# Kernel tuning notes

Hardware: AMD Instinct MI355X
Metric: run time of the kernel (lower is better)

Reference implementation:

```python
import jax, jax.numpy as jnp
import numpy as np

K = 8  # kNN fan-in (includes self at distance 0, matching torch_cluster.knn)


def _mlp2(x, w1, b1, w2, b2):
    # PyG MLP with plain_last=True: act between layers, none after last
    h = jax.nn.relu(x @ w1 + b1)
    return h @ w2 + b2


def _dynamic_edge_conv(x, w1, b1, w2, b2, k=K):
    # x: [B, N, C]. Recompute kNN graph from current features, EdgeConv with
    # message = MLP([x_i, x_j - x_i]) and max aggregation over neighbors.
    sq = jnp.sum(x * x, axis=-1)                                   # [B, N]
    d2 = sq[:, :, None] + sq[:, None, :] - 2.0 * jnp.einsum('bnc,bmc->bnm', x, x)
    _, idx = jax.lax.top_k(-d2, k)                                 # [B, N, k]
    xj = jax.vmap(lambda xx, ii: xx[ii])(x, idx)                   # [B, N, k, C]
    xi = jnp.broadcast_to(x[:, :, None, :], xj.shape)
    e = jnp.concatenate([xi, xj - xi], axis=-1)                    # [B, N, k, 2C]
    msg = _mlp2(e, w1, b1, w2, b2)                                 # [B, N, k, C_out]
    return jnp.max(msg, axis=2)                                    # [B, N, C_out]


def setup_inputs() -> dict:
    key = jax.random.key(0)
    ks = jax.random.split(key, 24)
    B, N = 2, 1000
    S = 0.05
    p = lambda i, shape: jax.random.normal(ks[i], shape, jnp.float32) * S
    return dict(
        pos=jax.random.normal(ks[0], (B, N, 3), jnp.float32),
        c1_w1=p(1, (6, 16)),   c1_b1=p(2, (16,)),  c1_w2=p(3, (16, 32)),   c1_b2=p(4, (32,)),
        c2_w1=p(5, (64, 64)),  c2_b1=p(6, (64,)),  c2_w2=p(7, (64, 128)),  c2_b2=p(8, (128,)),
        c3_w1=p(9, (256, 256)), c3_b1=p(10, (256,)), c3_w2=p(11, (256, 512)), c3_b2=p(12, (512,)),
        sm_w1=p(13, (672, 256)), sm_b1=p(14, (256,)), sm_w2=p(15, (256, 128)), sm_b2=p(16, (128,)),
        ec_w1=p(17, (384, 128)), ec_b1=p(18, (128,)), ec_w2=p(19, (128, 1)), ec_b2=p(20, (1,)),
    )


def reference(pos, c1_w1, c1_b1, c1_w2, c1_b2, c2_w1, c2_b1, c2_w2, c2_b2,
              c3_w1, c3_b1, c3_w2, c3_b2, sm_w1, sm_b1, sm_w2, sm_b2,
              ec_w1, ec_b1, ec_w2, ec_b2):
    x1 = _dynamic_edge_conv(pos, c1_w1, c1_b1, c1_w2, c1_b2)       # [B, N, 32]
    x2 = _dynamic_edge_conv(x1, c2_w1, c2_b1, c2_w2, c2_b2)        # [B, N, 128]
    x3 = _dynamic_edge_conv(x2, c3_w1, c3_b1, c3_w2, c3_b2)        # [B, N, 512]
    x = jnp.concatenate([x1, x2, x3], axis=-1)                     # [B, N, 672]
    sf = _mlp2(x, sm_w1, sm_b1, sm_w2, sm_b2)                      # [B, N, 128]
    g = jnp.max(sf, axis=1)                                        # [B, 128] global max pool

    N = pos.shape[1]
    t0, t1 = np.triu_indices(N, 1)                                 # 499500 pairs
    D = sf.shape[-1]
    # Linear(cat[feat_i, feat_j, global]) split into three small GEMMs on
    # [B,N,128] / [B,128] then gathered to pairs: identical math, avoids the
    # [B, P, 384] concat the torch code materializes.
    hi = sf @ ec_w1[:D]                                            # [B, N, 128]
    hj = sf @ ec_w1[D:2 * D]                                       # [B, N, 128]
    hg = g @ ec_w1[2 * D:] + ec_b1                                 # [B, 128]
    hidden = jax.nn.relu(hi[:, t0] + hj[:, t1] + hg[:, None, :])   # [B, P, 128]
    mlp_out = (hidden @ ec_w2 + ec_b2)[..., 0]                     # [B, P]
    pair_prob = jax.nn.sigmoid(mlp_out)
    return pair_prob, mlp_out
```

## Files before the change

kernel.cpp:

```cpp
#include <hip/hip_runtime.h>
#include <hip/hip_bf16.h>
#include <cmath>

#define NB 2
#define NP 1000
#define KNN 8
#define PPAIR 499500

typedef __hip_bfloat16 bf16;
typedef unsigned long long u64;
typedef unsigned short ushort;
typedef unsigned int uint;
typedef __attribute__((ext_vector_type(8))) short short8;
typedef __attribute__((ext_vector_type(4))) float f32x4;

__device__ __forceinline__ float b2f(bf16 v) { return __bfloat162float(v); }
__device__ __forceinline__ ushort f2b(float f) {
    uint x = __float_as_uint(f);
    return (ushort)((x + 0x7FFFu + ((x >> 16) & 1u)) >> 16);
}
__device__ __forceinline__ float ldin(const void* p, int flag, int i) {
    return flag ? ((const float*)p)[i] : b2f(((const bf16*)p)[i]);
}

#define OFF_POS    0
#define OFF_C1W1   6000
#define OFF_C1B1   6096
#define OFF_C1W2   6112
#define OFF_C1B2   6624
#define OFF_C2W1   6656
#define OFF_C2B1   10752
#define OFF_C2W2   10816
#define OFF_C2B2   19008
#define OFF_C3W1   19136
#define OFF_C3B1   84672
#define OFF_C3W2   84928
#define OFF_C3B2   216000
#define OFF_SMW1   216512
#define OFF_SMB1   388544
#define OFF_SMW2   388800
#define OFF_SMB2   421568
#define OFF_ECW1   421696
#define OFF_ECB1   470848
#define OFF_ECW2   470976
#define OFF_ECB2   471104
#define OFF_X1     471112
#define OFF_X2     535112
#define OFF_X3     791112
#define OFF_SF     1815112
#define OFF_G      2071112
#define OFF_HI     2071368
#define OFF_HJ     2327368
#define OFF_HG     2583368
#define OFF_FLAG   2583624
#define OFF_NIDX   2583632
#define OFF_GP     2599632
#define OFF_W1T    2606032
#define OFF_W2T    2638800
#define OFF_SMW1T  2704336
#define OFF_SMW2T  2790352
#define OFF_ECW1T  2806736
#define OFF_PL     2823120
#define OFF_E2W1T  3079120
#define OFF_E2W2T  3081168
#define OFF_D2     3085264

__global__ void detect_kernel(const void* pos, int* flag) {
    __shared__ float red[256];
    const unsigned short* p = (const unsigned short*)pos;
    float m = 0.f;
    for (int t = threadIdx.x; t < 6000; t += 256) {
        unsigned int u = ((unsigned int)p[t]) << 16;
        float v = fabsf(__uint_as_float(u));
        if (!isfinite(v)) v = 1e30f;
        m = fmaxf(m, v);
    }
    red[threadIdx.x] = m;
    __syncthreads();
    for (int s = 128; s > 0; s >>= 1) {
        if (threadIdx.x < s) red[threadIdx.x] = fmaxf(red[threadIdx.x], red[threadIdx.x + s]);
        __syncthreads();
    }
    if (threadIdx.x == 0) flag[0] = (red[0] > 1e6f) ? 1 : 0;
}

struct InPtrs { const void* p[21]; };

__global__ void cvt_all_kernel(InPtrs in, float* ws, const int* flag,
                               ushort* w1t, ushort* w2t, ushort* smw1t,
                               ushort* smw2t, ushort* ecw1t,
                               ushort* e2w1t, ushort* e2w2t) {
    const int sizes[21] = {6000, 96, 16, 512, 32, 4096, 64, 8192, 128,
                           65536, 256, 131072, 512, 172032, 256, 32768, 128,
                           49152, 128, 128, 1};
    const int offs[21] = {OFF_POS, OFF_C1W1, OFF_C1B1, OFF_C1W2, OFF_C1B2,
                          OFF_C2W1, OFF_C2B1, OFF_C2W2, OFF_C2B2,
                          OFF_C3W1, OFF_C3B1, OFF_C3W2, OFF_C3B2,
                          OFF_SMW1, OFF_SMB1, OFF_SMW2, OFF_SMB2,
                          OFF_ECW1, OFF_ECB1, OFF_ECW2, OFF_ECB2};
    int y = blockIdx.y;
    int t = blockIdx.x * 256 + threadIdx.x;
    int f = flag[0];
    if (y < 21) {
        if (t < sizes[y]) ws[offs[y] + t] = ldin(in.p[y], f, t);
    } else if (y == 21) {
        if (t < 65536) {
            int h = t >> 8, c = t & 255;
            w1t[t] = f2b(ldin(in.p[9], f, c * 256 + h));
        }
    } else if (y == 22) {
        if (t < 131072) {
            int o = t >> 8, h = t & 255;
            w2t[t] = f2b(ldin(in.p[11], f, h * 512 + o));
        }
    } else if (y == 23) {
        if (t < 172032) {
            int h = t / 672, c = t - h * 672;
            smw1t[t] = f2b(ldin(in.p[13], f, c * 256 + h));
        }
    } else if (y == 24) {
        if (t < 32768) {
            int o = t >> 8, h = t & 255;
            smw2t[t] = f2b(ldin(in.p[15], f, h * 128 + o));
        }
    } else if (y == 25) {
        if (t < 32768) {
            int op = t >> 7, c = t & 127;
            int idx = (op < 128) ? (c * 128 + op) : ((128 + c) * 128 + (op - 128));
            ecw1t[t] = f2b(ldin(in.p[17], f, idx));
        }
    } else if (y == 26) {
        if (t < 4096) {
            int h = t >> 6, c = t & 63;
            e2w1t[t] = f2b(ldin(in.p[5], f, c * 64 + h));
        }
    } else {
        if (t < 8192) {
            int o = t >> 6, h = t & 63;
            e2w2t[t] = f2b(ldin(in.p[7], f, h * 128 + o));
        }
    }
}

__device__ __forceinline__ void ce(u64& a, u64& b) {
    u64 lo = a < b ? a : b;
    u64 hi = a < b ? b : a;
    a = lo; b = hi;
}

__device__ __forceinline__ u64 umin64(u64 a, u64 b) { return a < b ? a : b; }

__device__ __forceinline__ void ins8(u64 (&best)[KNN], u64 cand) {
    u64 cur = cand;
    #pragma unroll
    for (int r = 0; r < KNN; ++r) {
        u64 lo = best[r] < cur ? best[r] : cur;
        u64 hi = best[r] < cur ? cur : best[r];
        best[r] = lo; cur = hi;
    }
}

__device__ __forceinline__ void merge4(u64 (&best)[KNN], u64 s0, u64 s1, u64 s2, u64 s3) {
    ce(s0, s1); ce(s2, s3); ce(s0, s2); ce(s1, s3); ce(s1, s2);
    best[4] = umin64(best[4], s3);
    best[5] = umin64(best[5], s2);
    best[6] = umin64(best[6], s1);
    best[7] = umin64(best[7], s0);
    ce(best[0], best[4]); ce(best[1], best[5]); ce(best[2], best[6]); ce(best[3], best[7]);
    ce(best[0], best[2]); ce(best[1], best[3]); ce(best[4], best[6]); ce(best[5], best[7]);
    ce(best[0], best[1]); ce(best[2], best[3]); ce(best[4], best[5]); ce(best[6], best[7]);
}

template <int C>
__global__ __launch_bounds__(256) void knn_fused_kernel(const float* __restrict__ x,
                                                        int* __restrict__ nidx) {
    constexpr int CP = (C + 3) & ~3;
    constexpr int PSTR = CP + 4;
    __shared__ float Qs[8 * PSTR];
    __shared__ float Ps[64 * PSTR];
    int tid = threadIdx.x;
    int b = blockIdx.y;
    int i0 = blockIdx.x * 8;
    int q = tid >> 5;
    int jcol = tid & 31;

    for (int idx = tid; idx < 8 * CP; idx += 256) {
        int row = idx / CP, c = idx % CP;
        int i = i0 + row;
        Qs[row * PSTR + c] = (c < C && i < NP) ? x[((size_t)b * NP + i) * C + c] : 0.f;
    }

    u64 best[KNN];
    #pragma unroll
    for (int r = 0; r < KNN; ++r) best[r] = ~0ull;

    for (int jc = 0; jc < 16; ++jc) {
        int j0 = jc * 64;
        __syncthreads();
        if (C % 4 == 0) {
            for (int idx = tid; idx < 64 * (C / 4); idx += 256) {
                int row = idx / (C / 4), c4 = idx % (C / 4);
                int j = j0 + row;
                float4 v = make_float4(0.f, 0.f, 0.f, 0.f);
                if (j < NP) v = *(const float4*)(x + ((size_t)b * NP + j) * C + c4 * 4);
                *(float4*)(&Ps[row * PSTR + c4 * 4]) = v;
            }
        } else {
            for (int idx = tid; idx < 64 * CP; idx += 256) {
                int row = idx / CP, c = idx % CP;
                int j = j0 + row;
                Ps[row * PSTR + c] = (c < C && j < NP) ? x[((size_t)b * NP + j) * C + c] : 0.f;
            }
        }
        __syncthreads();
        float d0 = 0.f, d1 = 0.f;
        #pragma unroll
        for (int c4 = 0; c4 < CP / 4; ++c4) {
            float4 qv = *(const float4*)(&Qs[q * PSTR + c4 * 4]);
            float4 p0 = *(const float4*)(&Ps[jcol * PSTR + c4 * 4]);
            float4 p1 = *(const float4*)(&Ps[(jcol + 32) * PSTR + c4 * 4]);
            float t;
            t = qv.x - p0.x; d0 += t * t;  t = qv.y - p0.y; d0 += t * t;
            t = qv.z - p0.z; d0 += t * t;  t = qv.w - p0.w; d0 += t * t;
            t = qv.x - p1.x; d1 += t * t;  t = qv.y - p1.y; d1 += t * t;
            t = qv.z - p1.z; d1 += t * t;  t = qv.w - p1.w; d1 += t * t;
        }
        int ja = j0 + jcol, jb = j0 + jcol + 32;
        u64 ca = (ja < NP) ? ((((u64)__float_as_uint(d0)) << 32) | (unsigned)ja) : ~0ull;
        u64 cb = (jb < NP) ? ((((u64)__float_as_uint(d1)) << 32) | (unsigned)jb) : ~0ull;
        ins8(best, ca);
        ins8(best, cb);
    }

    #pragma unroll
    for (int m = 1; m < 32; m <<= 1) {
        u64 other[KNN];
        #pragma unroll
        for (int r = 0; r < KNN; ++r)
            other[r] = __shfl_xor((unsigned long long)best[r], m, 64);
        u64 v[KNN];
        #pragma unroll
        for (int r = 0; r < KNN; ++r)
            v[r] = best[r] < other[7 - r] ? best[r] : other[7 - r];
        ce(v[0], v[4]); ce(v[1], v[5]); ce(v[2], v[6]); ce(v[3], v[7]);
        ce(v[0], v[2]); ce(v[1], v[3]); ce(v[4], v[6]); ce(v[5], v[7]);
        ce(v[0], v[1]); ce(v[2], v[3]); ce(v[4], v[5]); ce(v[6], v[7]);
        #pragma unroll
        for (int r = 0; r < KNN; ++r) best[r] = v[r];
    }

    int i = i0 + q;
    if (jcol == 0 && i < NP) {
        #pragma unroll
        for (int r = 0; r < KNN; ++r)
            nidx[((size_t)b * NP + i) * KNN + r] = (int)(best[r] & 0xffffffffu);
    }
}

template <int C>
__global__ __launch_bounds__(256) void dist_kernel(const float* __restrict__ x,
                                                   float* __restrict__ d2) {
    constexpr int CP = (C + 3) & ~3;
    constexpr int STR = CP + 4;
    __shared__ float As[32 * STR];
    __shared__ float Bs[64 * STR];
    int tid = threadIdx.x;
    int tx = tid & 31, ty = tid >> 5;
    int b = blockIdx.z;
    int i0 = blockIdx.x * 32;
    int j0 = blockIdx.y * 64;

    for (int idx = tid; idx < 32 * (CP / 4); idx += 256) {
        int row = idx / (CP / 4), c4 = idx % (CP / 4);
        int i = i0 + row;
        float4 v = make_float4(0.f, 0.f, 0.f, 0.f);
        if (i < NP) v = *(const float4*)(x + ((size_t)b * NP + i) * C + c4 * 4);
        *(float4*)(&As[row * STR + c4 * 4]) = v;
    }
    for (int idx = tid; idx < 64 * (CP / 4); idx += 256) {
        int row = idx / (CP / 4), c4 = idx % (CP / 4);
        int j = j0 + row;
        float4 v = make_float4(0.f, 0.f, 0.f, 0.f);
        if (j < NP) v = *(const float4*)(x + ((size_t)b * NP + j) * C + c4 * 4);
        *(float4*)(&Bs[row * STR + c4 * 4]) = v;
    }
    __syncthreads();

    float acc[4][2];
    #pragma unroll
    for (int r = 0; r < 4; ++r) { acc[r][0] = 0.f; acc[r][1] = 0.f; }
    #pragma unroll 4
    for (int k4 = 0; k4 < CP / 4; ++k4) {
        float4 b0 = *(const float4*)(&Bs[tx * STR + k4 * 4]);
        float4 b1 = *(const float4*)(&Bs[(tx + 32) * STR + k4 * 4]);
        #pragma unroll
        for (int r = 0; r < 4; ++r) {
            float4 a = *(const float4*)(&As[(ty * 4 + r) * STR + k4 * 4]);
            float d;
            d = a.x - b0.x; acc[r][0] += d * d;  d = a.x - b1.x; acc[r][1] += d * d;
            d = a.y - b0.y; acc[r][0] += d * d;  d = a.y - b1.y; acc[r][1] += d * d;
            d = a.z - b0.z; acc[r][0] += d * d;  d = a.z - b1.z; acc[r][1] += d * d;
            d = a.w - b0.w; acc[r][0] += d * d;  d = a.w - b1.w; acc[r][1] += d * d;
        }
    }

    int ja = j0 + tx, jb = j0 + tx + 32;
    #pragma unroll
    for (int r = 0; r < 4; ++r) {
        int i = i0 + ty * 4 + r;
        if (i < NP) {
            size_t base = ((size_t)b * NP + i) * NP;
            if (ja < NP) d2[base + ja] = acc[r][0];
            if (jb < NP) d2[base + jb] = acc[r][1];
        }
    }
}

__global__ __launch_bounds__(256) void knn_sel_kernel(const float* __restrict__ d2,
                                                      int* __restrict__ nidx) {
    int lane = threadIdx.x & 63;
    int q = blockIdx.x * 4 + (threadIdx.x >> 6);
    const float* row = d2 + (size_t)q * NP;
    u64 best[KNN];
    #pragma unroll
    for (int r = 0; r < KNN; ++r) best[r] = ~0ull;
    #pragma unroll
    for (int t = 0; t < 4; ++t) {
        int j = t * 256 + lane * 4;
        if (j < NP) {
            float4 v = *(const float4*)(row + j);
            merge4(best,
                   (((u64)__float_as_uint(v.x)) << 32) | (unsigned)(j + 0),
                   (((u64)__float_as_uint(v.y)) << 32) | (unsigned)(j + 1),
                   (((u64)__float_as_uint(v.z)) << 32) | (unsigned)(j + 2),
                   (((u64)__float_as_uint(v.w)) << 32) | (unsigned)(j + 3));
        }
    }
    #pragma unroll
    for (int m = 1; m < 64; m <<= 1) {
        u64 other[KNN];
        #pragma unroll
        for (int r = 0; r < KNN; ++r)
            other[r] = __shfl_xor((unsigned long long)best[r], m, 64);
        u64 v[KNN];
        #pragma unroll
        for (int r = 0; r < KNN; ++r)
            v[r] = umin64(best[r], other[KNN - 1 - r]);
        ce(v[0], v[4]); ce(v[1], v[5]); ce(v[2], v[6]); ce(v[3], v[7]);
        ce(v[0], v[2]); ce(v[1], v[3]); ce(v[4], v[6]); ce(v[5], v[7]);
        ce(v[0], v[1]); ce(v[2], v[3]); ce(v[4], v[5]); ce(v[6], v[7]);
        #pragma unroll
        for (int r = 0; r < KNN; ++r) best[r] = v[r];
    }
    if (lane == 0) {
        #pragma unroll
        for (int r = 0; r < KNN; ++r)
            nidx[(size_t)q * KNN + r] = (int)(best[r] & 0xffffffffu);
    }
}

template <int CIN, int CHID, int COUT>
__global__ void edgeconv_kernel(const float* __restrict__ x, const int* __restrict__ nidx,
                                const float* __restrict__ w1, const float* __restrict__ b1,
                                const float* __restrict__ w2, const float* __restrict__ b2,
                                float* __restrict__ y) {
    int bi = blockIdx.x;
    int b = bi / NP;
    __shared__ float xi[CIN];
    __shared__ float dx[KNN][CIN];
    __shared__ __align__(16) float hid[CHID][12];
    __shared__ int nb[KNN];
    int tid = threadIdx.x;
    if (tid < KNN) nb[tid] = nidx[bi * KNN + tid];
    for (int c = tid; c < CIN; c += 256) xi[c] = x[(size_t)bi * CIN + c];
    __syncthreads();
    for (int t = tid; t < KNN * CIN; t += 256) {
        int k = t / CIN, c = t % CIN;
        dx[k][c] = x[((size_t)b * NP + nb[k]) * CIN + c] - xi[c];
    }
    __syncthreads();
    for (int h = tid; h < CHID; h += 256) {
        float common = b1[h];
        for (int c = 0; c < CIN; ++c) common += xi[c] * w1[c * CHID + h];
        float acc[KNN];
        for (int k = 0; k < KNN; ++k) acc[k] = common;
        for (int c = 0; c < CIN; ++c) {
            float wv = w1[(CIN + c) * CHID + h];
            for (int k = 0; k < KNN; ++k) acc[k] += dx[k][c] * wv;
        }
        for (int k = 0; k < KNN; ++k) hid[h][k] = fmaxf(acc[k], 0.f);
    }
    __syncthreads();
    for (int o = tid; o < COUT; o += 256) {
        float acc[KNN];
        for (int k = 0; k < KNN; ++k) acc[k] = 0.f;
        for (int h = 0; h < CHID; ++h) {
            float wv = w2[h * COUT + o];
            float4 h0 = *(const float4*)&hid[h][0];
            float4 h1 = *(const float4*)&hid[h][4];
            acc[0] += h0.x * wv; acc[1] += h0.y * wv; acc[2] += h0.z * wv; acc[3] += h0.w * wv;
            acc[4] += h1.x * wv; acc[5] += h1.y * wv; acc[6] += h1.z * wv; acc[7] += h1.w * wv;
        }
        float m = acc[0];
        for (int k = 1; k < KNN; ++k) m = fmaxf(m, acc[k]);
        y[(size_t)bi * COUT + o] = m + b2[o];
    }
}

#define E2STR 72
__global__ __launch_bounds__(256) void ec2_mfma_kernel(
        const float* __restrict__ x1, const int* __restrict__ nidx,
        const ushort* __restrict__ w1t, const ushort* __restrict__ w2t,
        const float* __restrict__ b1f, const float* __restrict__ b2f,
        float* __restrict__ x2out) {
    __shared__ ushort Elds[32 * E2STR];
    __shared__ ushort Hlds[32 * E2STR];
    int tid = threadIdx.x;
    int P0 = blockIdx.x * 4;

    {
        int e = tid >> 3, seg = tid & 7;
        int bi = P0 + (e >> 3), k = e & 7;
        int b = bi / NP;
        int nb = nidx[bi * KNN + k];
        const float* xi = x1 + (size_t)bi * 32;
        const float* xj = x1 + ((size_t)b * NP + nb) * 32;
        int c0 = seg * 8;
        #pragma unroll
        for (int c = c0; c < c0 + 8; c += 4) {
            float4 v;
            if (c < 32) {
                v = *(const float4*)(xi + c);
            } else {
                float4 a = *(const float4*)(xi + c - 32);
                float4 q = *(const float4*)(xj + c - 32);
                v = make_float4(q.x - a.x, q.y - a.y, q.z - a.z, q.w - a.w);
            }
            uint lo = (uint)f2b(v.x) | ((uint)f2b(v.y) << 16);
            uint hi = (uint)f2b(v.z) | ((uint)f2b(v.w) << 16);
            *(uint2*)(&Elds[e * E2STR + c]) = make_uint2(lo, hi);
        }
    }
    __syncthreads();

    int lane = tid & 63, wave = tid >> 6;
    int n16 = lane & 15, quad = lane >> 4;

    {
        int nc = wave * 16;
        f32x4 acc[2];
        float bv = b1f[nc + n16];
        acc[0] = (f32x4){bv, bv, bv, bv};
        acc[1] = acc[0];
        #pragma unroll
        for (int k8 = 0; k8 < 2; ++k8) {
            int ko = k8 * 32 + quad * 8;
            short8 a0 = *(const short8*)(&Elds[(n16) * E2STR + ko]);
            short8 a1 = *(const short8*)(&Elds[(16 + n16) * E2STR + ko]);
            short8 bfr = *(const short8*)(&w1t[(size_t)(nc + n16) * 64 + ko]);
            acc[0] = __builtin_amdgcn_mfma_f32_16x16x32_bf16(a0, bfr, acc[0], 0, 0, 0);
            acc[1] = __builtin_amdgcn_mfma_f32_16x16x32_bf16(a1, bfr, acc[1], 0, 0, 0);
        }
        #pragma unroll
        for (int mt = 0; mt < 2; ++mt) {
            int col = nc + n16;
            #pragma unroll
            for (int r = 0; r < 4; ++r) {
                int row = mt * 16 + quad * 4 + r;
                Hlds[row * E2STR + col] = f2b(fmaxf(acc[mt][r], 0.f));
            }
        }
    }
    __syncthreads();

    {
        int nc2 = wave * 32;
        f32x4 acc[2][2];
        #pragma unroll
        for (int mt = 0; mt < 2; ++mt)
            #pragma unroll
            for (int nt = 0; nt < 2; ++nt) acc[mt][nt] = (f32x4){0.f, 0.f, 0.f, 0.f};
        #pragma unroll
        for (int k8 = 0; k8 < 2; ++k8) {
            int ko = k8 * 32 + quad * 8;
            short8 a0 = *(const short8*)(&Hlds[(n16) * E2STR + ko]);
            short8 a1 = *(const short8*)(&Hlds[(16 + n16) * E2STR + ko]);
            #pragma unroll
            for (int nt = 0; nt < 2; ++nt) {
                short8 bfr = *(const short8*)(&w2t[(size_t)(nc2 + nt * 16 + n16) * 64 + ko]);
                acc[0][nt] = __builtin_amdgcn_mfma_f32_16x16x32_bf16(a0, bfr, acc[0][nt], 0, 0, 0);
                acc[1][nt] = __builtin_amdgcn_mfma_f32_16x16x32_bf16(a1, bfr, acc[1][nt], 0, 0, 0);
            }
        }
        #pragma unroll
        for (int mt = 0; mt < 2; ++mt)
            #pragma unroll
            for (int nt = 0; nt < 2; ++nt) {
                f32x4 a = acc[mt][nt];
                float v = fmaxf(fmaxf(a[0], a[1]), fmaxf(a[2], a[3]));
                float o = fmaxf(v, __shfl_xor(v, 16, 64));
                int col = nc2 + nt * 16 + n16;
                if (quad == 0)
                    x2out[(size_t)(P0 + mt * 2) * 128 + col] = o + b2f[col];
                else if (quad == 2)
                    x2out[(size_t)(P0 + mt * 2 + 1) * 128 + col] = o + b2f[col];
            }
    }
}

#define ESTR 264
__global__ __launch_bounds__(256) void ec3_mfma_kernel(
        const float* __restrict__ x2, const int* __restrict__ nidx,
        const ushort* __restrict__ w1t, const ushort* __restrict__ w2t,
        const float* __restrict__ b1f, const float* __restrict__ b2f,
        float* __restrict__ x3) {
    __shared__ ushort Elds[32 * ESTR];
    __shared__ ushort Hlds[32 * ESTR];
    int tid = threadIdx.x;
    int P0 = blockIdx.x * 4;

    {
        int e = tid >> 3, seg = tid & 7;
        int bi = P0 + (e >> 3), k = e & 7;
        int b = bi / NP;
        int nb = nidx[bi * KNN + k];
        const float* xi = x2 + (size_t)bi * 128;
        const float* xj = x2 + ((size_t)b * NP + nb) * 128;
        int c0 = seg * 16;
        #pragma unroll
        for (int c = c0; c < c0 + 16; c += 4) {
            float4 a = *(const float4*)(xi + c);
            float4 q = *(const float4*)(xj + c);
            uint lo = (uint)f2b(a.x) | ((uint)f2b(a.y) << 16);
            uint hi = (uint)f2b(a.z) | ((uint)f2b(a.w) << 16);
            *(uint2*)(&Elds[e * ESTR + c]) = make_uint2(lo, hi);
            lo = (uint)f2b(q.x - a.x) | ((uint)f2b(q.y - a.y) << 16);
            hi = (uint)f2b(q.z - a.z) | ((uint)f2b(q.w - a.w) << 16);
            *(uint2*)(&Elds[e * ESTR + 128 + c]) = make_uint2(lo, hi);
        }
    }
    __syncthreads();

    int lane = tid & 63, wave = tid >> 6;
    int n16 = lane & 15, quad = lane >> 4;

    {
        int nc = wave * 64;
        f32x4 acc1[2][4];
        #pragma unroll
        for (int mt = 0; mt < 2; ++mt)
            #pragma unroll
            for (int nt = 0; nt < 4; ++nt) {
                float bv = b1f[nc + nt * 16 + n16];
                acc1[mt][nt] = (f32x4){bv, bv, bv, bv};
            }
        #pragma unroll
        for (int k8 = 0; k8 < 8; ++k8) {
            int ko = k8 * 32 + quad * 8;
            short8 a0 = *(const short8*)(&Elds[(n16) * ESTR + ko]);
            short8 a1 = *(const short8*)(&Elds[(16 + n16) * ESTR + ko]);
            #pragma unroll
            for (int nt = 0; nt < 4; ++nt) {
                short8 bfr = *(const short8*)(&w1t[(size_t)(nc + nt * 16 + n16) * 256 + ko]);
                acc1[0][nt] = __builtin_amdgcn_mfma_f32_16x16x32_bf16(a0, bfr, acc1[0][nt], 0, 0, 0);
                acc1[1][nt] = __builtin_amdgcn_mfma_f32_16x16x32_bf16(a1, bfr, acc1[1][nt], 0, 0, 0);
            }
        }
        #pragma unroll
        for (int mt = 0; mt < 2; ++mt)
            #pragma unroll
            for (int nt = 0; nt < 4; ++nt) {
                int col = nc + nt * 16 + n16;
                #pragma unroll
                for (int r = 0; r < 4; ++r) {
                    int row = mt * 16 + quad * 4 + r;
                    Hlds[row * ESTR + col] = f2b(fmaxf(acc1[mt][nt][r], 0.f));
                }
            }
    }
    __syncthreads();

    {
        int nc2 = wave * 128;
        f32x4 acc2[2][8];
        #pragma unroll
        for (int mt = 0; mt < 2; ++mt)
            #pragma unroll
            for (int nt = 0; nt < 8; ++nt) acc2[mt][nt] = (f32x4){0.f, 0.f, 0.f, 0.f};
        #pragma unroll
        for (int k8 = 0; k8 < 8; ++k8) {
            int ko = k8 * 32 + quad * 8;
            short8 a0 = *(const short8*)(&Hlds[(n16) * ESTR + ko]);
            short8 a1 = *(const short8*)(&Hlds[(16 + n16) * ESTR + ko]);
            #pragma unroll
            for (int nt = 0; nt < 8; ++nt) {
                short8 bfr = *(const short8*)(&w2t[(size_t)(nc2 + nt * 16 + n16) * 256 + ko]);
                acc2[0][nt] = __builtin_amdgcn_mfma_f32_16x16x32_bf16(a0, bfr, acc2[0][nt], 0, 0, 0);
                acc2[1][nt] = __builtin_amdgcn_mfma_f32_16x16x32_bf16(a1, bfr, acc2[1][nt], 0, 0, 0);
            }
        }
        #pragma unroll
        for (int mt = 0; mt < 2; ++mt)
            #pragma unroll
            for (int nt = 0; nt < 8; ++nt) {
                f32x4 a = acc2[mt][nt];
                float v = fmaxf(fmaxf(a[0], a[1]), fmaxf(a[2], a[3]));
                float o = fmaxf(v, __shfl_xor(v, 16, 64));
                int col = nc2 + nt * 16 + n16;
                if (quad == 0)
                    x3[(size_t)(P0 + mt * 2) * 512 + col] = o + b2f[col];
                else if (quad == 2)
                    x3[(size_t)(P0 + mt * 2 + 1) * 512 + col] = o + b2f[col];
            }
    }
}

#define XSTR 680
#define SSTR 136
__global__ __launch_bounds__(256) void sm_mfma_kernel(
        const float* __restrict__ x1, const float* __restrict__ x2,
        const float* __restrict__ x3,
        const ushort* __restrict__ w1t, const ushort* __restrict__ w2t,
        const ushort* __restrict__ ecw1t,
        const float* __restrict__ b1f, const float* __restrict__ b2f,
        float* __restrict__ sf, float* __restrict__ hi, float* __restrict__ hj) {
    __shared__ ushort Xlds[32 * XSTR];
    __shared__ ushort Hlds[32 * ESTR];
    __shared__ ushort Slds[32 * SSTR];
    int tid = threadIdx.x;
    int P0 = blockIdx.x * 32;

    {
        int row = tid >> 3, cseg = tid & 7;
        int p = P0 + row;
        bool ok = p < NB * NP;
        #pragma unroll
        for (int k = 0; k < 21; ++k) {
            int c = cseg * 4 + k * 32;
            float4 v = make_float4(0.f, 0.f, 0.f, 0.f);
            if (ok) {
                if (c < 32) v = *(const float4*)(x1 + (size_t)p * 32 + c);
                else if (c < 160) v = *(const float4*)(x2 + (size_t)p * 128 + (c - 32));
                else v = *(const float4*)(x3 + (size_t)p * 512 + (c - 160));
            }
            uint lo = (uint)f2b(v.x) | ((uint)f2b(v.y) << 16);
            uint hv = (uint)f2b(v.z) | ((uint)f2b(v.w) << 16);
            *(uint2*)(&Xlds[row * XSTR + c]) = make_uint2(lo, hv);
        }
    }
    __syncthreads();

    int lane = tid & 63, wave = tid >> 6;
    int n16 = lane & 15, quad = lane >> 4;

    {
        int nc = wave * 64;
        f32x4 acc[2][4];
        #pragma unroll
        for (int mt = 0; mt < 2; ++mt)
            #pragma unroll
            for (int nt = 0; nt < 4; ++nt) {
                float bv = b1f[nc + nt * 16 + n16];
                acc[mt][nt] = (f32x4){bv, bv, bv, bv};
            }
        #pragma unroll
        for (int k8 = 0; k8 < 21; ++k8) {
            int ko = k8 * 32 + quad * 8;
            short8 a0 = *(const short8*)(&Xlds[(n16) * XSTR + ko]);
            short8 a1 = *(const short8*)(&Xlds[(16 + n16) * XSTR + ko]);
            #pragma unroll
            for (int nt = 0; nt < 4; ++nt) {
                short8 bfr = *(const short8*)(&w1t[(size_t)(nc + nt * 16 + n16) * 672 + ko]);
                acc[0][nt] = __builtin_amdgcn_mfma_f32_16x16x32_bf16(a0, bfr, acc[0][nt], 0, 0, 0);
                acc[1][nt] = __builtin_amdgcn_mfma_f32_16x16x32_bf16(a1, bfr, acc[1][nt], 0, 0, 0);
            }
        }
        #pragma unroll
        for (int mt = 0; mt < 2; ++mt)
            #pragma unroll
            for (int nt = 0; nt < 4; ++nt) {
                int col = nc + nt * 16 + n16;
                #pragma unroll
                for (int r = 0; r < 4; ++r) {
                    int row = mt * 16 + quad * 4 + r;
                    Hlds[row * ESTR + col] = f2b(fmaxf(acc[mt][nt][r], 0.f));
                }
            }
    }
    __syncthreads();

    {
        int nc = wave * 32;
        f32x4 acc[2][2];
        #pragma unroll
        for (int mt = 0; mt < 2; ++mt)
            #pragma unroll
            for (int nt = 0; nt < 2; ++nt) {
                float bv = b2f[nc + nt * 16 + n16];
                acc[mt][nt] = (f32x4){bv, bv, bv, bv};
            }
        #pragma unroll
        for (int k8 = 0; k8 < 8; ++k8) {
            int ko = k8 * 32 + quad * 8;
            short8 a0 = *(const short8*)(&Hlds[(n16) * ESTR + ko]);
            short8 a1 = *(const short8*)(&Hlds[(16 + n16) * ESTR + ko]);
            #pragma unroll
            for (int nt = 0; nt < 2; ++nt) {
                short8 bfr = *(const short8*)(&w2t[(size_t)(nc + nt * 16 + n16) * 256 + ko]);
                acc[0][nt] = __builtin_amdgcn_mfma_f32_16x16x32_bf16(a0, bfr, acc[0][nt], 0, 0, 0);
                acc[1][nt] = __builtin_amdgcn_mfma_f32_16x16x32_bf16(a1, bfr, acc[1][nt], 0, 0, 0);
            }
        }
        #pragma unroll
        for (int mt = 0; mt < 2; ++mt)
            #pragma unroll
            for (int nt = 0; nt < 2; ++nt) {
                int col = nc + nt * 16 + n16;
                #pragma unroll
                for (int r = 0; r < 4; ++r) {
                    int row = mt * 16 + quad * 4 + r;
                    int p = P0 + row;
                    float v = acc[mt][nt][r];
                    if (p < NB * NP) sf[(size_t)p * 128 + col] = v;
                    Slds[row * SSTR + col] = f2b(v);
                }
            }
    }
    __syncthreads();

    {
        int nc = wave * 64;
        f32x4 acc[2][4];
        #pragma unroll
        for (int mt = 0; mt < 2; ++mt)
            #pragma unroll
            for (int nt = 0; nt < 4; ++nt) acc[mt][nt] = (f32x4){0.f, 0.f, 0.f, 0.f};
        #pragma unroll
        for (int k8 = 0; k8 < 4; ++k8) {
            int ko = k8 * 32 + quad * 8;
            short8 a0 = *(const short8*)(&Slds[(n16) * SSTR + ko]);
            short8 a1 = *(const short8*)(&Slds[(16 + n16) * SSTR + ko]);
            #pragma unroll
            for (int nt = 0; nt < 4; ++nt) {
                short8 bfr = *(const short8*)(&ecw1t[(size_t)(nc + nt * 16 + n16) * 128 + ko]);
                acc[0][nt] = __builtin_amdgcn_mfma_f32_16x16x32_bf16(a0, bfr, acc[0][nt], 0, 0, 0);
                acc[1][nt] = __builtin_amdgcn_mfma_f32_16x16x32_bf16(a1, bfr, acc[1][nt], 0, 0, 0);
            }
        }
        #pragma unroll
        for (int mt = 0; mt < 2; ++mt)
            #pragma unroll
            for (int nt = 0; nt < 4; ++nt) {
                int colp = nc + nt * 16 + n16;
                float* dst = (colp < 128) ? hi : hj;
                int col = colp & 127;
                #pragma unroll
                for (int r = 0; r < 4; ++r) {
                    int row = mt * 16 + quad * 4 + r;
                    int p = P0 + row;
                    if (p < NB * NP) dst[(size_t)p * 128 + col] = acc[mt][nt][r];
                }
            }
    }
}

__global__ void gmax1_kernel(const float* __restrict__ sf, float* __restrict__ part) {
    int m = blockIdx.x;
    int b = m / 25, ch = m % 25, o = threadIdx.x;
    float v = -INFINITY;
    int n0 = ch * 40;
    for (int n = n0; n < n0 + 40; ++n)
        v = fmaxf(v, sf[((size_t)b * NP + n) * 128 + o]);
    part[(size_t)m * 128 + o] = v;
}

__global__ void gfin_kernel(const float* __restrict__ part, const float* __restrict__ w1,
                            const float* __restrict__ b1, float* __restrict__ hg) {
    int b = blockIdx.x, o = threadIdx.x;
    __shared__ float gs[128];
    float v = -INFINITY;
    for (int ch = 0; ch < 25; ++ch)
        v = fmaxf(v, part[((size_t)b * 25 + ch) * 128 + o]);
    gs[o] = v;
    __syncthreads();
    float acc = b1[o];
    for (int c = 0; c < 128; ++c) acc += gs[c] * w1[(256 + c) * 128 + o];
    hg[b * 128 + o] = acc;
}

__global__ __launch_bounds__(256) void pair_kernel(
        const float* __restrict__ hi, const float* __restrict__ hj,
        const float* __restrict__ hg,
        const float* __restrict__ w2, const float* __restrict__ b2,
        void* __restrict__ out, const int* __restrict__ flag) {
    int j0 = blockIdx.x * 32, i0 = blockIdx.y * 32, b = blockIdx.z;
    if (j0 + 31 <= i0) return;
    __shared__ float hit[32][132];
    __shared__ float hjt[32][132];
    __shared__ __align__(16) float w2s[128];
    int tid = threadIdx.x;
    if (tid < 128) w2s[tid] = w2[tid];
    for (int t = tid; t < 32 * 128; t += 256) {
        int r = t >> 7, c = t & 127;
        int i = i0 + r, j = j0 + r;
        hit[r][c] = (i < NP) ? hi[((size_t)b * NP + i) * 128 + c] : 0.f;
        hjt[r][c] = ((j < NP) ? hj[((size_t)b * NP + j) * 128 + c] : 0.f) + hg[b * 128 + c];
    }
    __syncthreads();
    float bb = b2[0];
    int f = flag[0];
    int tj = tid & 31;
    int ti0 = tid >> 5;
    int j = j0 + tj;
    float acc[4] = {0.f, 0.f, 0.f, 0.f};
    #pragma unroll 4
    for (int o4 = 0; o4 < 32; ++o4) {
        float4 hv = *(const float4*)(&hjt[tj][o4 * 4]);
        float4 wv = *(const float4*)(&w2s[o4 * 4]);
        #pragma unroll
        for (int r = 0; r < 4; ++r) {
            float4 a = *(const float4*)(&hit[ti0 + 8 * r][o4 * 4]);
            acc[r] += fmaxf(a.x + hv.x, 0.f) * wv.x
                    + fmaxf(a.y + hv.y, 0.f) * wv.y
                    + fmaxf(a.z + hv.z, 0.f) * wv.z
                    + fmaxf(a.w + hv.w, 0.f) * wv.w;
        }
    }
    #pragma unroll
    for (int r = 0; r < 4; ++r) {
        int i = i0 + ti0 + 8 * r;
        if (i < j && j < NP) {
            size_t p = (size_t)i * (NP - 1) - (size_t)i * (i - 1) / 2 + (j - i - 1);
            float mo = acc[r] + bb;
            float pr = 1.f / (1.f + expf(-mo));
            size_t idx0 = (size_t)b * PPAIR + p;
            size_t idx1 = (size_t)NB * PPAIR + idx0;
            if (f) {
                ((float*)out)[idx0] = pr;
                ((float*)out)[idx1] = mo;
            } else {
                ((bf16*)out)[idx0] = __float2bfloat16(pr);
                ((bf16*)out)[idx1] = __float2bfloat16(mo);
            }
        }
    }
}

extern "C" void kernel_launch(void* const* d_in, const int* in_sizes, int n_in,
                              void* d_out, int out_size, void* d_ws, size_t ws_size,
                              hipStream_t stream) {
    float* ws = (float*)d_ws;
    float* posf = ws + OFF_POS;
    float* x1   = ws + OFF_X1;
    float* x2   = ws + OFF_X2;
    float* x3   = ws + OFF_X3;
    float* sf   = ws + OFF_SF;
    float* hi   = ws + OFF_HI;
    float* hj   = ws + OFF_HJ;
    float* hgb  = ws + OFF_HG;
    int*   flag = (int*)(ws + OFF_FLAG);
    int*   nidx = (int*)(ws + OFF_NIDX);
    float* gp   = ws + OFF_GP;
    float* d2m  = ws + OFF_D2;
    ushort* w1t = (ushort*)(ws + OFF_W1T);
    ushort* w2t = (ushort*)(ws + OFF_W2T);
    ushort* smw1t = (ushort*)(ws + OFF_SMW1T);
    ushort* smw2t = (ushort*)(ws + OFF_SMW2T);
    ushort* ecw1t = (ushort*)(ws + OFF_ECW1T);
    ushort* e2w1t = (ushort*)(ws + OFF_E2W1T);
    ushort* e2w2t = (ushort*)(ws + OFF_E2W2T);

    detect_kernel<<<1, 256, 0, stream>>>(d_in[0], flag);

    InPtrs ip;
    for (int i = 0; i < 21; ++i) ip.p[i] = d_in[i];
    dim3 cgrid(672, 28);
    cvt_all_kernel<<<cgrid, 256, 0, stream>>>(ip, ws, flag, w1t, w2t, smw1t, smw2t,
                                              ecw1t, e2w1t, e2w2t);

    dim3 kgrid_f(NP / 8, NB);
    dim3 dgrid(32, 16, 2);
    int selgrid = NB * NP / 4;

    knn_fused_kernel<3><<<kgrid_f, 256, 0, stream>>>(posf, nidx);
    edgeconv_kernel<3, 16, 32><<<NB * NP, 256, 0, stream>>>(
        posf, nidx, ws + OFF_C1W1, ws + OFF_C1B1, ws + OFF_C1W2, ws + OFF_C1B2, x1);

    dist_kernel<32><<<dgrid, 256, 0, stream>>>(x1, d2m);
    knn_sel_kernel<<<selgrid, 256, 0, stream>>>(d2m, nidx);
    ec2_mfma_kernel<<<NB * NP / 4, 256, 0, stream>>>(
        x1, nidx, e2w1t, e2w2t, ws + OFF_C2B1, ws + OFF_C2B2, x2);

    dist_kernel<128><<<dgrid, 256, 0, stream>>>(x2, d2m);
    knn_sel_kernel<<<selgrid, 256, 0, stream>>>(d2m, nidx);
    ec3_mfma_kernel<<<NB * NP / 4, 256, 0, stream>>>(
        x2, nidx, w1t, w2t, ws + OFF_C3B1, ws + OFF_C3B2, x3);

    sm_mfma_kernel<<<(NB * NP + 31) / 32, 256, 0, stream>>>(
        x1, x2, x3, smw1t, smw2t, ecw1t, ws + OFF_SMB1, ws + OFF_SMB2, sf, hi, hj);

    gmax1_kernel<<<NB * 25, 128, 0, stream>>>(sf, gp);
    gfin_kernel<<<NB, 128, 0, stream>>>(gp, ws + OFF_ECW1, ws + OFF_ECB1, hgb);

    dim3 pgrid(32, 32, NB);
    pair_kernel<<<pgrid, 256, 0, stream>>>(hi, hj, hgb, ws + OFF_ECW2, ws + OFF_ECB2,
                                           d_out, flag);
}
```

Measured before the change: 286.9 us.

## Widen pair tile to 32x64 with 4x2 register blocking and prefetch

The pair kernel tile grows from 32x32 to 32x64 pairs. Each thread now computes a 4x2 register block, so every shared-memory load of hi and hj is reused across more pairs. The inner loop double-buffers the LDS loads by hand, and the shared-memory fill uses float4 loads. This cuts LDS traffic and block count per pair, at the cost of more registers, larger shared memory, and more wasted work in diagonal tiles.

```diff
diff --git a/kernel.cpp b/kernel.cpp
--- a/kernel.cpp
+++ b/kernel.cpp
@@ -788,59 +788,97 @@
     hg[b * 128 + o] = acc;
 }
 
+#define PLD(o4, A_, H0_, H1_, W_)                                              \
+    {                                                                          \
+        W_  = *(const float4*)(&w2s[(o4) * 4]);                                \
+        H0_ = *(const float4*)(&hjt[tj][(o4) * 4]);                            \
+        H1_ = *(const float4*)(&hjt[tj + 32][(o4) * 4]);                       \
+        _Pragma("unroll")                                                      \
+        for (int r = 0; r < 4; ++r)                                            \
+            A_[r] = *(const float4*)(&hit[ti3 * 4 + r][(o4) * 4]);             \
+    }
+#define PCOMP(A_, H0_, H1_, W_)                                                \
+    {                                                                          \
+        _Pragma("unroll")                                                      \
+        for (int r = 0; r < 4; ++r) {                                          \
+            float4 a = A_[r];                                                  \
+            acc[r][0] += fmaxf(a.x + H0_.x, 0.f) * W_.x                        \
+                       + fmaxf(a.y + H0_.y, 0.f) * W_.y                        \
+                       + fmaxf(a.z + H0_.z, 0.f) * W_.z                        \
+                       + fmaxf(a.w + H0_.w, 0.f) * W_.w;                       \
+            acc[r][1] += fmaxf(a.x + H1_.x, 0.f) * W_.x                        \
+                       + fmaxf(a.y + H1_.y, 0.f) * W_.y                        \
+                       + fmaxf(a.z + H1_.z, 0.f) * W_.z                        \
+                       + fmaxf(a.w + H1_.w, 0.f) * W_.w;                       \
+        }                                                                      \
+    }
+
 __global__ __launch_bounds__(256) void pair_kernel(
         const float* __restrict__ hi, const float* __restrict__ hj,
         const float* __restrict__ hg,
         const float* __restrict__ w2, const float* __restrict__ b2,
         void* __restrict__ out, const int* __restrict__ flag) {
-    int j0 = blockIdx.x * 32, i0 = blockIdx.y * 32, b = blockIdx.z;
-    if (j0 + 31 <= i0) return;
+    int j0 = blockIdx.x * 64, i0 = blockIdx.y * 32, b = blockIdx.z;
+    if (j0 + 63 <= i0) return;
     __shared__ float hit[32][132];
-    __shared__ float hjt[32][132];
+    __shared__ float hjt[64][132];
     __shared__ __align__(16) float w2s[128];
     int tid = threadIdx.x;
     if (tid < 128) w2s[tid] = w2[tid];
-    for (int t = tid; t < 32 * 128; t += 256) {
-        int r = t >> 7, c = t & 127;
-        int i = i0 + r, j = j0 + r;
-        hit[r][c] = (i < NP) ? hi[((size_t)b * NP + i) * 128 + c] : 0.f;
-        hjt[r][c] = ((j < NP) ? hj[((size_t)b * NP + j) * 128 + c] : 0.f) + hg[b * 128 + c];
-    }
-    __syncthreads();
+    int c4 = tid & 31;
+    float4 hgv = *(const float4*)(hg + b * 128 + c4 * 4);
+    for (int t = tid; t < 96 * 32; t += 256) {
+        int row = t >> 5;
+        if (row < 32) {
+            int i = i0 + row;
+            float4 v = make_float4(0.f, 0.f, 0.f, 0.f);
+            if (i < NP) v = *(const float4*)(hi + ((size_t)b * NP + i) * 128 + c4 * 4);
+            *(float4*)(&hit[row][c4 * 4]) = v;
+        } else {
+            int j = j0 + row - 32;
+            float4 v = make_float4(0.f, 0.f, 0.f, 0.f);
+            if (j < NP) v = *(const float4*)(hj + ((size_t)b * NP + j) * 128 + c4 * 4);
+            *(float4*)(&hjt[row - 32][c4 * 4]) =
+                make_float4(v.x + hgv.x, v.y + hgv.y, v.z + hgv.z, v.w + hgv.w);
+        }
+    }
+    __syncthreads();
+
+    int tj = tid & 31;
+    int ti3 = tid >> 5;
+    float acc[4][2] = {{0.f, 0.f}, {0.f, 0.f}, {0.f, 0.f}, {0.f, 0.f}};
+
+    float4 A0[4], H00, H01, W0;
+    float4 A1[4], H10, H11, W1;
+    PLD(0, A0, H00, H01, W0)
+    for (int o = 0; o < 32; o += 2) {
+        PLD(o + 1, A1, H10, H11, W1)
+        PCOMP(A0, H00, H01, W0)
+        if (o + 2 < 32) PLD(o + 2, A0, H00, H01, W0)
+        PCOMP(A1, H10, H11, W1)
+    }
+
     float bb = b2[0];
     int f = flag[0];
-    int tj = tid & 31;
-    int ti0 = tid >> 5;
-    int j = j0 + tj;
-    float acc[4] = {0.f, 0.f, 0.f, 0.f};
-    #pragma unroll 4
-    for (int o4 = 0; o4 < 32; ++o4) {
-        float4 hv = *(const float4*)(&hjt[tj][o4 * 4]);
-        float4 wv = *(const float4*)(&w2s[o4 * 4]);
-        #pragma unroll
-        for (int r = 0; r < 4; ++r) {
-            float4 a = *(const float4*)(&hit[ti0 + 8 * r][o4 * 4]);
-            acc[r] += fmaxf(a.x + hv.x, 0.f) * wv.x
-                    + fmaxf(a.y + hv.y, 0.f) * wv.y
-                    + fmaxf(a.z + hv.z, 0.f) * wv.z
-                    + fmaxf(a.w + hv.w, 0.f) * wv.w;
-        }
-    }
     #pragma unroll
     for (int r = 0; r < 4; ++r) {
-        int i = i0 + ti0 + 8 * r;
-        if (i < j && j < NP) {
-            size_t p = (size_t)i * (NP - 1) - (size_t)i * (i - 1) / 2 + (j - i - 1);
-            float mo = acc[r] + bb;
-            float pr = 1.f / (1.f + expf(-mo));
-            size_t idx0 = (size_t)b * PPAIR + p;
-            size_t idx1 = (size_t)NB * PPAIR + idx0;
-            if (f) {
-                ((float*)out)[idx0] = pr;
-                ((float*)out)[idx1] = mo;
-            } else {
-                ((bf16*)out)[idx0] = __float2bfloat16(pr);
-                ((bf16*)out)[idx1] = __float2bfloat16(mo);
+        int i = i0 + ti3 * 4 + r;
+        #pragma unroll
+        for (int jj = 0; jj < 2; ++jj) {
+            int j = j0 + tj + jj * 32;
+            if (i < j && j < NP) {
+                size_t p = (size_t)i * (NP - 1) - (size_t)i * (i - 1) / 2 + (j - i - 1);
+                float mo = acc[r][jj] + bb;
+                float pr = 1.f / (1.f + expf(-mo));
+                size_t idx0 = (size_t)b * PPAIR + p;
+                size_t idx1 = (size_t)NB * PPAIR + idx0;
+                if (f) {
+                    ((float*)out)[idx0] = pr;
+                    ((float*)out)[idx1] = mo;
+                } else {
+                    ((bf16*)out)[idx0] = __float2bfloat16(pr);
+                    ((bf16*)out)[idx1] = __float2bfloat16(mo);
+                }
             }
         }
     }
@@ -902,7 +940,7 @@
     gmax1_kernel<<<NB * 25, 128, 0, stream>>>(sf, gp);
     gfin_kernel<<<NB, 128, 0, stream>>>(gp, ws + OFF_ECW1, ws + OFF_ECB1, hgb);
 
-    dim3 pgrid(32, 32, NB);
+    dim3 pgrid(16, 32, NB);
     pair_kernel<<<pgrid, 256, 0, stream>>>(hi, hj, hgb, ws + OFF_ECW2, ws + OFF_ECB2,
                                            d_out, flag);
 }
```

New measurement: 278.3 us. -3.0%, faster.
